# Optimization experiments

Hardware: AMD Instinct MI355X
Metric: run time of the kernel (lower is better)

The kernel has to match this reference:

```python
import jax, jax.numpy as jnp
import numpy as np

B, N, C = 8, 1024, 768
H = 12
HD = C // H
RANK = 8
SCALE = HD ** -0.5


def setup_inputs() -> dict:
    key = jax.random.key(0)
    ks = jax.random.split(key, 12)
    s = C ** -0.5
    inp = {
        'x': jax.random.normal(ks[0], (B, N, C), jnp.float32),
        'w_qkv': jax.random.normal(ks[1], (3 * C, C), jnp.float32) * s,
        'b_qkv': jax.random.normal(ks[2], (3 * C,), jnp.float32) * 0.02,
        'w_proj': jax.random.normal(ks[3], (C, C), jnp.float32) * s,
        'b_proj': jax.random.normal(ks[4], (C,), jnp.float32) * 0.02,
        # LoRA A matrices (kaiming-uniform-ish); B matrices are zero at init,
        # but use small nonzero values so the adapter path is exercised.
        'q_a': jax.random.normal(ks[5], (RANK, C), jnp.float32) * s,
        'q_b': jax.random.normal(ks[6], (C, RANK), jnp.float32) * 0.01,
        'k_a': jax.random.normal(ks[7], (RANK, C), jnp.float32) * s,
        'k_b': jax.random.normal(ks[8], (C, RANK), jnp.float32) * 0.01,
        'v_a': jax.random.normal(ks[9], (RANK, C), jnp.float32) * s,
        'v_b': jax.random.normal(ks[10], (C, RANK), jnp.float32) * 0.01,
        'o_a': jax.random.normal(ks[11], (RANK, C), jnp.float32) * s,
        'o_b': jax.random.normal(jax.random.fold_in(key, 99), (C, RANK), jnp.float32) * 0.01,
    }
    return inp


def _lora(x, wa, wb):
    # x:[B,N,C], wa:[r,C], wb:[C,r] -> [B,N,C]
    return jnp.einsum('bnr,cr->bnc', jnp.einsum('bnc,rc->bnr', x, wa), wb)


def reference(x, w_qkv, b_qkv, w_proj, b_proj, q_a, q_b, k_a, k_b, v_a, v_b, o_a, o_b):
    # QKV projection + fused LoRA slice-adds
    qkv = jnp.einsum('bnc,dc->bnd', x, w_qkv) + b_qkv  # [B,N,3C]
    q = qkv[:, :, :C] + _lora(x, q_a, q_b)
    k = qkv[:, :, C:2 * C] + _lora(x, k_a, k_b)
    v = qkv[:, :, 2 * C:] + _lora(x, v_a, v_b)
    # [B,H,N,HD]
    q = q.reshape(B, N, H, HD).transpose(0, 2, 1, 3)
    k = k.reshape(B, N, H, HD).transpose(0, 2, 1, 3)
    v = v.reshape(B, N, H, HD).transpose(0, 2, 1, 3)
    attn = jnp.einsum('bhqd,bhkd->bhqk', q, k) * SCALE
    attn = jax.nn.softmax(attn, axis=-1)  # dropout is identity in eval
    o = jnp.einsum('bhqk,bhkd->bhqd', attn, v)
    o = o.transpose(0, 2, 1, 3).reshape(B, N, C)
    out = jnp.einsum('bnc,dc->bnd', o, w_proj) + b_proj + _lora(o, o_a, o_b)
    return out
```

## Files before the change

kernel.cpp:

```cpp
#include <hip/hip_runtime.h>

typedef __attribute__((ext_vector_type(8))) short short8;
typedef __attribute__((ext_vector_type(4))) float f32x4;
typedef __attribute__((ext_vector_type(4))) unsigned short u16x4;
typedef __attribute__((ext_vector_type(2))) unsigned int u32x2;

#define MFMA16(a,b,c) __builtin_amdgcn_mfma_f32_16x16x32_bf16((a),(b),(c),0,0,0)

#define QSCALE 0.1803368801f

__device__ __forceinline__ unsigned short f2bf(float f) {
  unsigned int x = __float_as_uint(f);
  x += 0x7fffu + ((x >> 16) & 1u);
  return (unsigned short)(x >> 16);
}
__device__ __forceinline__ unsigned int pack2bf(float a, float b) {
  unsigned int ua = __float_as_uint(a) + 0x8000u;
  unsigned int ub = __float_as_uint(b) + 0x8000u;
  return __builtin_amdgcn_perm(ub, ua, 0x07060302);
}
__device__ __forceinline__ void gload16(const unsigned short* g, unsigned short* l) {
  __builtin_amdgcn_global_load_lds(
      (const __attribute__((address_space(1))) unsigned int*)g,
      (__attribute__((address_space(3))) unsigned int*)l, 16, 0, 0);
}


__global__ __launch_bounds__(256) void prep(
    const float* __restrict__ x,
    const float* __restrict__ w_qkv,
    const float* __restrict__ w_proj,
    const float* __restrict__ q_a, const float* __restrict__ q_b,
    const float* __restrict__ k_a, const float* __restrict__ k_b,
    const float* __restrict__ v_a, const float* __restrict__ v_b,
    const float* __restrict__ o_a, const float* __restrict__ o_b,
    unsigned short* __restrict__ xf,
    unsigned short* __restrict__ wqkv_eff,
    unsigned short* __restrict__ wproj_eff)
{
  int bid = blockIdx.x;
  if (bid < 6144) {
    int i4 = (bid * 256 + threadIdx.x) * 4;
    int m  = i4 / 768;
    int k4 = i4 - m * 768;
    f32x4 v = *(const f32x4*)&x[i4];
    u16x4 o;
    o.x = f2bf(v.x); o.y = f2bf(v.y); o.z = f2bf(v.z); o.w = f2bf(v.w);
    int kb = k4 >> 5, qd = (k4 >> 3) & 3, j0 = k4 & 7;
    size_t idx = ((size_t)(kb * 512 + (m >> 4)) << 9) +
                 (((qd << 4) + (m & 15)) << 3) + j0;
    *(u16x4*)&xf[idx] = o;
    return;
  }
  const int QKV = 2304 * 768;
  int idx = (bid - 6144) * 256 + threadIdx.x;
  if (idx < QKV) {
    int n = idx / 768, c = idx - n * 768;
    int sec = n / 768;
    int nr = n - sec * 768;
    const float* a; const float* b;
    if (sec == 0)      { a = q_a; b = q_b; }
    else if (sec == 1) { a = k_a; b = k_b; }
    else               { a = v_a; b = v_b; }
    float acc = w_qkv[idx];
    #pragma unroll
    for (int r = 0; r < 8; r++)
      acc += b[nr * 8 + r] * a[r * 768 + c];
    wqkv_eff[idx] = f2bf(acc);
  } else {
    int i2 = idx - QKV;
    int n = i2 / 768, c = i2 - n * 768;
    float acc = w_proj[i2];
    #pragma unroll
    for (int r = 0; r < 8; r++)
      acc += o_b[n * 8 + r] * o_a[r * 768 + c];
    wproj_eff[i2] = f2bf(acc);
  }
}

__global__ __launch_bounds__(256) void gemm_bt(
    const unsigned short* __restrict__ Af,
    const unsigned short* __restrict__ W,
    const float* __restrict__ bias,
    unsigned short* __restrict__ out0,
    unsigned short* __restrict__ out1,
    unsigned short* __restrict__ out2,
    float* __restrict__ outf,
    int K, int Ncols, int mode)
{
  __shared__ alignas(16) unsigned short Ws[64][72];
  const int tid  = threadIdx.x;
  const int wave = tid >> 6;
  const int lane = tid & 63;
  const int quad = lane >> 4;
  const int l16  = lane & 15;
  const int m0 = blockIdx.x * 128;
  const int n0 = blockIdx.y * 64;
  const int M16b = (m0 >> 4) + wave * 2;

  int wr[2], wc[2];
  #pragma unroll
  for (int i = 0; i < 2; i++) { int f = tid + i * 256; wr[i] = f >> 3; wc[i] = (f & 7) << 3; }

  f32x4 wreg[2];
  #pragma unroll
  for (int i = 0; i < 2; i++)
    wreg[i] = *(const f32x4*)&W[(size_t)(n0 + wr[i]) * K + wc[i]];

  short8 aCur[2][2], aNxt[2][2] = {};
  #pragma unroll
  for (int t = 0; t < 2; t++)
    #pragma unroll
    for (int ks = 0; ks < 2; ks++)
      aCur[t][ks] = *(const short8*)&Af[((size_t)(ks * 512 + M16b + t) << 9) + (lane << 3)];

  f32x4 acc[2][4] = {};

  for (int k0 = 0; k0 < K; k0 += 64) {
    __syncthreads();
    #pragma unroll
    for (int i = 0; i < 2; i++) *(f32x4*)&Ws[wr[i]][wc[i]] = wreg[i];
    __syncthreads();
    if (k0 + 64 < K) {
      #pragma unroll
      for (int i = 0; i < 2; i++)
        wreg[i] = *(const f32x4*)&W[(size_t)(n0 + wr[i]) * K + k0 + 64 + wc[i]];
      const int kbn = (k0 + 64) >> 5;
      #pragma unroll
      for (int t = 0; t < 2; t++)
        #pragma unroll
        for (int ks = 0; ks < 2; ks++)
          aNxt[t][ks] = *(const short8*)&Af[((size_t)((kbn + ks) * 512 + M16b + t) << 9) + (lane << 3)];
    }
    #pragma unroll
    for (int ks = 0; ks < 2; ks++) {
      const int kk = ks * 32 + quad * 8;
      short8 b0 = *(const short8*)&Ws[l16][kk];
      short8 b1 = *(const short8*)&Ws[16 + l16][kk];
      short8 b2 = *(const short8*)&Ws[32 + l16][kk];
      short8 b3 = *(const short8*)&Ws[48 + l16][kk];
      acc[0][0] = MFMA16(aCur[0][ks], b0, acc[0][0]);
      acc[0][1] = MFMA16(aCur[0][ks], b1, acc[0][1]);
      acc[0][2] = MFMA16(aCur[0][ks], b2, acc[0][2]);
      acc[0][3] = MFMA16(aCur[0][ks], b3, acc[0][3]);
      acc[1][0] = MFMA16(aCur[1][ks], b0, acc[1][0]);
      acc[1][1] = MFMA16(aCur[1][ks], b1, acc[1][1]);
      acc[1][2] = MFMA16(aCur[1][ks], b2, acc[1][2]);
      acc[1][3] = MFMA16(aCur[1][ks], b3, acc[1][3]);
    }
    #pragma unroll
    for (int t = 0; t < 2; t++)
      #pragma unroll
      for (int ks = 0; ks < 2; ks++)
        aCur[t][ks] = aNxt[t][ks];
  }

  float bv[4];
  #pragma unroll
  for (int j = 0; j < 4; j++) bv[j] = bias[n0 + j * 16 + l16];

  if (mode == 0) {
    const int sec = n0 / 768;
    const int h   = (n0 % 768) >> 6;
    unsigned short* dst = (sec == 0) ? out0 : ((sec == 1) ? out1 : out2);
    const float scl = (sec == 0) ? QSCALE : 1.0f;
    #pragma unroll
    for (int rg = 0; rg < 2; rg++) {
      #pragma unroll
      for (int r = 0; r < 4; r++) {
        int m  = m0 + wave * 32 + rg * 16 + quad * 4 + r;
        int b  = m >> 10, np = m & 1023;
        int bh = b * 12 + h;
        int npp = (np & ~63) | ((np & 15) * 4 + ((np >> 4) & 3));
        #pragma unroll
        for (int j = 0; j < 4; j++) {
          int d = j * 16 + l16;
          float v = (acc[rg][j][r] + bv[j]) * scl;
          if (sec < 2) dst[((size_t)bh << 16) + ((size_t)np << 6) + d] = f2bf(v);
          else         dst[((size_t)bh << 16) + ((size_t)d << 10) + npp] = f2bf(v);
        }
      }
    }
  } else {
    #pragma unroll
    for (int rg = 0; rg < 2; rg++) {
      #pragma unroll
      for (int r = 0; r < 4; r++) {
        int m = m0 + wave * 32 + rg * 16 + quad * 4 + r;
        #pragma unroll
        for (int j = 0; j < 4; j++)
          outf[(size_t)m * Ncols + n0 + j * 16 + l16] = acc[rg][j][r] + bv[j];
      }
    }
  }
}

__global__ __launch_bounds__(256) void attn(
    const unsigned short* __restrict__ q,
    const unsigned short* __restrict__ k,
    const unsigned short* __restrict__ vt,
    unsigned short* __restrict__ of)
{
  __shared__ alignas(16) unsigned short Qs[128][72];
  __shared__ alignas(16) unsigned short Ks2[2][64 * 64];
  __shared__ alignas(16) unsigned short Vs2[2][64 * 64];
  const int tid  = threadIdx.x;
  const int wave = tid >> 6;
  const int lane = tid & 63;
  const int quad = lane >> 4;
  const int l16  = lane & 15;
  const int bh = blockIdx.x;
  const int q0 = blockIdx.y * 128;
  const unsigned short* qb = q  + ((size_t)bh << 16);
  const unsigned short* kb = k  + ((size_t)bh << 16);
  const unsigned short* vb = vt + ((size_t)bh << 16);

  const int lrow   = lane >> 3;
  const int lchunk = (lane & 7) ^ lrow;
  const unsigned short* gK[2];
  const unsigned short* gV[2];
  int lsKV[2];
  #pragma unroll
  for (int t = 0; t < 2; t++) {
    int rr = wave * 16 + t * 8 + lrow;
    gK[t]   = kb + (size_t)rr * 64 + lchunk * 8;
    gV[t]   = vb + (size_t)rr * 1024 + lchunk * 8;
    lsKV[t] = rr * 64 + (lane & 7) * 8;
  }
  const int swz = l16 & 7;

  #pragma unroll
  for (int t = 0; t < 2; t++) {
    gload16(gK[t], &Ks2[0][lsKV[t]]);
    gload16(gV[t], &Vs2[0][lsKV[t]]);
  }

  #pragma unroll
  for (int i = 0; i < 4; i++) {
    int flat = tid + i * 256;
    int r = flat >> 3, ck = (flat & 7) << 3;
    *(f32x4*)&Qs[r][ck] = *(const f32x4*)&qb[((size_t)(q0 + r) << 6) + ck];
  }
  __syncthreads();
  short8 aq[2][2];
  #pragma unroll
  for (int rg = 0; rg < 2; rg++)
    #pragma unroll
    for (int ks = 0; ks < 2; ks++)
      aq[rg][ks] = *(const short8*)&Qs[wave * 32 + rg * 16 + l16][ks * 32 + quad * 8];
  unsigned short (*Ps)[72] = (unsigned short (*)[72])(&Qs[wave * 32][0]);

  f32x4 Oacc[2][4] = {};
  float lsum[2][4] = {};

  for (int kt = 0; kt < 16; kt++) {
    const int p = kt & 1;
    __syncthreads();
    if (kt < 15) {
      #pragma unroll
      for (int t = 0; t < 2; t++) {
        gload16(gK[t] + (kt + 1) * 4096, &Ks2[1 - p][lsKV[t]]);
        gload16(gV[t] + (kt + 1) * 64,   &Vs2[1 - p][lsKV[t]]);
      }
    }

    f32x4 s[2][4] = {};
    #pragma unroll
    for (int ks = 0; ks < 2; ks++) {
      const int cs = ks * 4 + quad;
      short8 b0 = *(const short8*)&Ks2[p][(l16)      * 64 + ((cs ^ swz) << 3)];
      short8 b1 = *(const short8*)&Ks2[p][(16 + l16) * 64 + ((cs ^ swz) << 3)];
      short8 b2 = *(const short8*)&Ks2[p][(32 + l16) * 64 + ((cs ^ swz) << 3)];
      short8 b3 = *(const short8*)&Ks2[p][(48 + l16) * 64 + ((cs ^ swz) << 3)];
      s[0][0] = MFMA16(aq[0][ks], b0, s[0][0]);
      s[0][1] = MFMA16(aq[0][ks], b1, s[0][1]);
      s[0][2] = MFMA16(aq[0][ks], b2, s[0][2]);
      s[0][3] = MFMA16(aq[0][ks], b3, s[0][3]);
      s[1][0] = MFMA16(aq[1][ks], b0, s[1][0]);
      s[1][1] = MFMA16(aq[1][ks], b1, s[1][1]);
      s[1][2] = MFMA16(aq[1][ks], b2, s[1][2]);
      s[1][3] = MFMA16(aq[1][ks], b3, s[1][3]);
    }

    #pragma unroll
    for (int rg = 0; rg < 2; rg++) {
      #pragma unroll
      for (int r = 0; r < 4; r++) {
        float p0 = exp2f(s[rg][0][r]);
        float p1 = exp2f(s[rg][1][r]);
        float p2 = exp2f(s[rg][2][r]);
        float p3 = exp2f(s[rg][3][r]);
        lsum[rg][r] += (p0 + p1) + (p2 + p3);
        u32x2 pk;
        pk.x = pack2bf(p0, p1);
        pk.y = pack2bf(p2, p3);
        *(u32x2*)&Ps[rg * 16 + quad * 4 + r][4 * l16] = pk;
      }
    }

    #pragma unroll
    for (int ks = 0; ks < 2; ks++) {
      const int kk = ks * 32 + quad * 8;
      const int cs = ks * 4 + quad;
      short8 a0 = *(const short8*)&Ps[l16][kk];
      short8 a1 = *(const short8*)&Ps[16 + l16][kk];
      short8 v0 = *(const short8*)&Vs2[p][(l16)      * 64 + ((cs ^ swz) << 3)];
      short8 v1 = *(const short8*)&Vs2[p][(16 + l16) * 64 + ((cs ^ swz) << 3)];
      short8 v2 = *(const short8*)&Vs2[p][(32 + l16) * 64 + ((cs ^ swz) << 3)];
      short8 v3 = *(const short8*)&Vs2[p][(48 + l16) * 64 + ((cs ^ swz) << 3)];
      Oacc[0][0] = MFMA16(a0, v0, Oacc[0][0]);
      Oacc[0][1] = MFMA16(a0, v1, Oacc[0][1]);
      Oacc[0][2] = MFMA16(a0, v2, Oacc[0][2]);
      Oacc[0][3] = MFMA16(a0, v3, Oacc[0][3]);
      Oacc[1][0] = MFMA16(a1, v0, Oacc[1][0]);
      Oacc[1][1] = MFMA16(a1, v1, Oacc[1][1]);
      Oacc[1][2] = MFMA16(a1, v2, Oacc[1][2]);
      Oacc[1][3] = MFMA16(a1, v3, Oacc[1][3]);
    }
  }

  const int b = bh / 12, h = bh - (bh / 12) * 12;
  #pragma unroll
  for (int rg = 0; rg < 2; rg++) {
    #pragma unroll
    for (int r = 0; r < 4; r++) {
      float t = lsum[rg][r];
      t += __shfl_xor(t, 1, 64);
      t += __shfl_xor(t, 2, 64);
      t += __shfl_xor(t, 4, 64);
      t += __shfl_xor(t, 8, 64);
      float inv = 1.0f / t;
      int np  = q0 + wave * 32 + rg * 16 + quad * 4 + r;
      int M16 = b * 64 + (np >> 4);
      int l16m = np & 15;
      #pragma unroll
      for (int j = 0; j < 4; j++) {
        int col = h * 64 + j * 16 + l16;
        int kb2 = col >> 5;
        int qc  = (col >> 3) & 3;
        size_t idx = ((size_t)(kb2 * 512 + M16) << 9) +
                     ((qc * 16 + l16m) << 3) + (l16 & 7);
        of[idx] = f2bf(Oacc[rg][j][r] * inv);
      }
    }
  }
}

extern "C" void kernel_launch(void* const* d_in, const int* in_sizes, int n_in,
                              void* d_out, int out_size, void* d_ws, size_t ws_size,
                              hipStream_t stream) {
  const float* x      = (const float*)d_in[0];
  const float* w_qkv  = (const float*)d_in[1];
  const float* b_qkv  = (const float*)d_in[2];
  const float* w_proj = (const float*)d_in[3];
  const float* b_proj = (const float*)d_in[4];
  const float* q_a    = (const float*)d_in[5];
  const float* q_b    = (const float*)d_in[6];
  const float* k_a    = (const float*)d_in[7];
  const float* k_b    = (const float*)d_in[8];
  const float* v_a    = (const float*)d_in[9];
  const float* v_b    = (const float*)d_in[10];
  const float* o_a    = (const float*)d_in[11];
  const float* o_b    = (const float*)d_in[12];

  char* ws = (char*)d_ws;
  unsigned short* wqkv_eff  = (unsigned short*)(ws + 0);
  unsigned short* wproj_eff = (unsigned short*)(ws + 3538944);
  unsigned short* xf        = (unsigned short*)(ws + 4718592);
  unsigned short* qd        = (unsigned short*)(ws + 17301504);
  unsigned short* kd        = (unsigned short*)(ws + 29884416);
  unsigned short* vtd       = (unsigned short*)(ws + 42467328);
  unsigned short* of        = xf;

  prep<<<dim3(6144 + 9216), dim3(256), 0, stream>>>(
      x, w_qkv, w_proj, q_a, q_b, k_a, k_b, v_a, v_b, o_a, o_b,
      xf, wqkv_eff, wproj_eff);

  gemm_bt<<<dim3(64, 36), dim3(256), 0, stream>>>(
      xf, wqkv_eff, b_qkv, qd, kd, vtd, nullptr, 768, 2304, 0);

  attn<<<dim3(96, 8), dim3(256), 0, stream>>>(qd, kd, vtd, of);

  gemm_bt<<<dim3(64, 12), dim3(256), 0, stream>>>(
      of, wproj_eff, b_proj, nullptr, nullptr, nullptr, (float*)d_out, 768, 768, 1);
}
```

Baseline: 233.5 us.

## Compute transposed scores so P stays in registers, dropping LDS round-trip

The QK^T product is computed as K·Q^T (K rows as the A operand, Q as the B operand, loaded straight from global), so each lane's score fragment already matches the A-operand layout needed for the PV MFMA. This removes the Q staging buffer in LDS and the store and reload of P through shared memory. The V-transpose permutation in the QKV epilogue is changed to match the new key ordering, and the row-sum reduction is reworked around the transposed layout. s_setprio is also raised around the MFMA blocks. LDS use drops and occupancy may rise, at the cost of a more delicate index permutation that must stay consistent across both kernels.

```diff
diff --git a/kernel.cpp b/kernel.cpp
--- a/kernel.cpp
+++ b/kernel.cpp
@@ -4,6 +4,7 @@
 typedef __attribute__((ext_vector_type(4))) float f32x4;
 typedef __attribute__((ext_vector_type(4))) unsigned short u16x4;
 typedef __attribute__((ext_vector_type(2))) unsigned int u32x2;
+typedef __attribute__((ext_vector_type(4))) unsigned int u32x4;
 
 #define MFMA16(a,b,c) __builtin_amdgcn_mfma_f32_16x16x32_bf16((a),(b),(c),0,0,0)
 
@@ -171,7 +172,7 @@
         int m  = m0 + wave * 32 + rg * 16 + quad * 4 + r;
         int b  = m >> 10, np = m & 1023;
         int bh = b * 12 + h;
-        int npp = (np & ~63) | ((np & 15) * 4 + ((np >> 4) & 3));
+        int npp = (np & ~63) | (np & 35) | ((np & 12) << 1) | ((np & 16) >> 2);
         #pragma unroll
         for (int j = 0; j < 4; j++) {
           int d = j * 16 + l16;
@@ -201,7 +202,6 @@
     const unsigned short* __restrict__ vt,
     unsigned short* __restrict__ of)
 {
-  __shared__ alignas(16) unsigned short Qs[128][72];
   __shared__ alignas(16) unsigned short Ks2[2][64 * 64];
   __shared__ alignas(16) unsigned short Vs2[2][64 * 64];
   const int tid  = threadIdx.x;
@@ -235,23 +235,18 @@
     gload16(gV[t], &Vs2[0][lsKV[t]]);
   }
 
-  #pragma unroll
-  for (int i = 0; i < 4; i++) {
-    int flat = tid + i * 256;
-    int r = flat >> 3, ck = (flat & 7) << 3;
-    *(f32x4*)&Qs[r][ck] = *(const f32x4*)&qb[((size_t)(q0 + r) << 6) + ck];
-  }
-  __syncthreads();
-  short8 aq[2][2];
+  short8 bq[2][2];
   #pragma unroll
   for (int rg = 0; rg < 2; rg++)
     #pragma unroll
     for (int ks = 0; ks < 2; ks++)
-      aq[rg][ks] = *(const short8*)&Qs[wave * 32 + rg * 16 + l16][ks * 32 + quad * 8];
-  unsigned short (*Ps)[72] = (unsigned short (*)[72])(&Qs[wave * 32][0]);
+      bq[rg][ks] = *(const short8*)&qb[((size_t)(q0 + wave * 32 + rg * 16 + l16) << 6) +
+                                       ks * 32 + quad * 8];
 
   f32x4 Oacc[2][4] = {};
-  float lsum[2][4] = {};
+  float lsum[2] = {};
+
+  union PAW { u32x4 w; short8 h; };
 
   for (int kt = 0; kt < 16; kt++) {
     const int p = kt & 1;
@@ -264,59 +259,79 @@
       }
     }
 
-    f32x4 s[2][4] = {};
+    f32x4 s[4][2] = {};
     #pragma unroll
     for (int ks = 0; ks < 2; ks++) {
       const int cs = ks * 4 + quad;
-      short8 b0 = *(const short8*)&Ks2[p][(l16)      * 64 + ((cs ^ swz) << 3)];
-      short8 b1 = *(const short8*)&Ks2[p][(16 + l16) * 64 + ((cs ^ swz) << 3)];
-      short8 b2 = *(const short8*)&Ks2[p][(32 + l16) * 64 + ((cs ^ swz) << 3)];
-      short8 b3 = *(const short8*)&Ks2[p][(48 + l16) * 64 + ((cs ^ swz) << 3)];
-      s[0][0] = MFMA16(aq[0][ks], b0, s[0][0]);
-      s[0][1] = MFMA16(aq[0][ks], b1, s[0][1]);
-      s[0][2] = MFMA16(aq[0][ks], b2, s[0][2]);
-      s[0][3] = MFMA16(aq[0][ks], b3, s[0][3]);
-      s[1][0] = MFMA16(aq[1][ks], b0, s[1][0]);
-      s[1][1] = MFMA16(aq[1][ks], b1, s[1][1]);
-      s[1][2] = MFMA16(aq[1][ks], b2, s[1][2]);
-      s[1][3] = MFMA16(aq[1][ks], b3, s[1][3]);
-    }
-
+      short8 a0 = *(const short8*)&Ks2[p][(l16)      * 64 + ((cs ^ swz) << 3)];
+      short8 a1 = *(const short8*)&Ks2[p][(16 + l16) * 64 + ((cs ^ swz) << 3)];
+      short8 a2 = *(const short8*)&Ks2[p][(32 + l16) * 64 + ((cs ^ swz) << 3)];
+      short8 a3 = *(const short8*)&Ks2[p][(48 + l16) * 64 + ((cs ^ swz) << 3)];
+      __builtin_amdgcn_s_setprio(1);
+      s[0][0] = MFMA16(a0, bq[0][ks], s[0][0]);
+      s[0][1] = MFMA16(a0, bq[1][ks], s[0][1]);
+      s[1][0] = MFMA16(a1, bq[0][ks], s[1][0]);
+      s[1][1] = MFMA16(a1, bq[1][ks], s[1][1]);
+      s[2][0] = MFMA16(a2, bq[0][ks], s[2][0]);
+      s[2][1] = MFMA16(a2, bq[1][ks], s[2][1]);
+      s[3][0] = MFMA16(a3, bq[0][ks], s[3][0]);
+      s[3][1] = MFMA16(a3, bq[1][ks], s[3][1]);
+      __builtin_amdgcn_s_setprio(0);
+    }
+
+    short8 pa[2][2];
     #pragma unroll
     for (int rg = 0; rg < 2; rg++) {
-      #pragma unroll
-      for (int r = 0; r < 4; r++) {
-        float p0 = exp2f(s[rg][0][r]);
-        float p1 = exp2f(s[rg][1][r]);
-        float p2 = exp2f(s[rg][2][r]);
-        float p3 = exp2f(s[rg][3][r]);
-        lsum[rg][r] += (p0 + p1) + (p2 + p3);
-        u32x2 pk;
-        pk.x = pack2bf(p0, p1);
-        pk.y = pack2bf(p2, p3);
-        *(u32x2*)&Ps[rg * 16 + quad * 4 + r][4 * l16] = pk;
+      f32x4 e[4];
+      #pragma unroll
+      for (int i = 0; i < 4; i++) {
+        e[i].x = exp2f(s[i][rg].x);
+        e[i].y = exp2f(s[i][rg].y);
+        e[i].z = exp2f(s[i][rg].z);
+        e[i].w = exp2f(s[i][rg].w);
+      }
+      lsum[rg] += (((e[0].x + e[0].y) + (e[0].z + e[0].w)) +
+                   ((e[1].x + e[1].y) + (e[1].z + e[1].w))) +
+                  (((e[2].x + e[2].y) + (e[2].z + e[2].w)) +
+                   ((e[3].x + e[3].y) + (e[3].z + e[3].w)));
+      #pragma unroll
+      for (int ks = 0; ks < 2; ks++) {
+        PAW pw;
+        pw.w.x = pack2bf(e[2 * ks].x,     e[2 * ks].y);
+        pw.w.y = pack2bf(e[2 * ks].z,     e[2 * ks].w);
+        pw.w.z = pack2bf(e[2 * ks + 1].x, e[2 * ks + 1].y);
+        pw.w.w = pack2bf(e[2 * ks + 1].z, e[2 * ks + 1].w);
+        pa[rg][ks] = pw.h;
       }
     }
 
     #pragma unroll
     for (int ks = 0; ks < 2; ks++) {
-      const int kk = ks * 32 + quad * 8;
       const int cs = ks * 4 + quad;
-      short8 a0 = *(const short8*)&Ps[l16][kk];
-      short8 a1 = *(const short8*)&Ps[16 + l16][kk];
       short8 v0 = *(const short8*)&Vs2[p][(l16)      * 64 + ((cs ^ swz) << 3)];
       short8 v1 = *(const short8*)&Vs2[p][(16 + l16) * 64 + ((cs ^ swz) << 3)];
       short8 v2 = *(const short8*)&Vs2[p][(32 + l16) * 64 + ((cs ^ swz) << 3)];
       short8 v3 = *(const short8*)&Vs2[p][(48 + l16) * 64 + ((cs ^ swz) << 3)];
-      Oacc[0][0] = MFMA16(a0, v0, Oacc[0][0]);
-      Oacc[0][1] = MFMA16(a0, v1, Oacc[0][1]);
-      Oacc[0][2] = MFMA16(a0, v2, Oacc[0][2]);
-      Oacc[0][3] = MFMA16(a0, v3, Oacc[0][3]);
-      Oacc[1][0] = MFMA16(a1, v0, Oacc[1][0]);
-      Oacc[1][1] = MFMA16(a1, v1, Oacc[1][1]);
-      Oacc[1][2] = MFMA16(a1, v2, Oacc[1][2]);
-      Oacc[1][3] = MFMA16(a1, v3, Oacc[1][3]);
-    }
+      __builtin_amdgcn_s_setprio(1);
+      Oacc[0][0] = MFMA16(pa[0][ks], v0, Oacc[0][0]);
+      Oacc[0][1] = MFMA16(pa[0][ks], v1, Oacc[0][1]);
+      Oacc[0][2] = MFMA16(pa[0][ks], v2, Oacc[0][2]);
+      Oacc[0][3] = MFMA16(pa[0][ks], v3, Oacc[0][3]);
+      Oacc[1][0] = MFMA16(pa[1][ks], v0, Oacc[1][0]);
+      Oacc[1][1] = MFMA16(pa[1][ks], v1, Oacc[1][1]);
+      Oacc[1][2] = MFMA16(pa[1][ks], v2, Oacc[1][2]);
+      Oacc[1][3] = MFMA16(pa[1][ks], v3, Oacc[1][3]);
+      __builtin_amdgcn_s_setprio(0);
+    }
+  }
+
+  float red[2];
+  #pragma unroll
+  for (int rg = 0; rg < 2; rg++) {
+    float t = lsum[rg];
+    t += __shfl_xor(t, 16, 64);
+    t += __shfl_xor(t, 32, 64);
+    red[rg] = t;
   }
 
   const int b = bh / 12, h = bh - (bh / 12) * 12;
@@ -324,12 +339,7 @@
   for (int rg = 0; rg < 2; rg++) {
     #pragma unroll
     for (int r = 0; r < 4; r++) {
-      float t = lsum[rg][r];
-      t += __shfl_xor(t, 1, 64);
-      t += __shfl_xor(t, 2, 64);
-      t += __shfl_xor(t, 4, 64);
-      t += __shfl_xor(t, 8, 64);
-      float inv = 1.0f / t;
+      float inv = 1.0f / __shfl(red[rg], (lane & 48) | (quad * 4 + r), 64);
       int np  = q0 + wave * 32 + rg * 16 + quad * 4 + r;
       int M16 = b * 64 + (np >> 4);
       int l16m = np & 15;
```

After: 236.2 us. No clear change (+1.2%).
